# Kernel optimization log

Hardware: AMD Instinct MI355X
Metric: run time of the kernel (lower is better)

The kernel has to match this reference:

```python
import jax, jax.numpy as jnp
import numpy as np

EMB = 1024
HEADS = 16
HEAD_SZ = 64
INNER = 4 * EMB
EPS = 1e-5


def layer_norm(x, g, b):
    mu = jnp.mean(x, axis=-1, keepdims=True)
    var = jnp.mean(jnp.square(x - mu), axis=-1, keepdims=True)
    return (x - mu) * jax.lax.rsqrt(var + EPS) * g + b


def setup_inputs() -> dict:
    key = jax.random.key(0)
    ks = jax.random.split(key, 12)
    s = 1.0 / np.sqrt(EMB)
    si = 1.0 / np.sqrt(INNER)
    return {
        "x": jax.random.normal(ks[0], (4, 2048, EMB), dtype=jnp.float32),
        "Wq": jax.random.uniform(ks[1], (EMB, HEADS * HEAD_SZ), jnp.float32, -s, s),
        "Wk": jax.random.uniform(ks[2], (EMB, HEADS * HEAD_SZ), jnp.float32, -s, s),
        "Wv": jax.random.uniform(ks[3], (EMB, HEADS * HEAD_SZ), jnp.float32, -s, s),
        "Wo": jax.random.uniform(ks[4], (HEADS * HEAD_SZ, EMB), jnp.float32, -s, s),
        "bo": jax.random.uniform(ks[5], (EMB,), jnp.float32, -s, s),
        "g1": jnp.ones((EMB,), jnp.float32),
        "b1": jnp.zeros((EMB,), jnp.float32),
        "W1": jax.random.uniform(ks[6], (EMB, INNER), jnp.float32, -s, s),
        "bf1": jax.random.uniform(ks[7], (INNER,), jnp.float32, -s, s),
        "W2": jax.random.uniform(ks[8], (INNER, EMB), jnp.float32, -si, si),
        "bf2": jax.random.uniform(ks[9], (EMB,), jnp.float32, -si, si),
        "g2": jnp.ones((EMB,), jnp.float32),
        "b2": jnp.zeros((EMB,), jnp.float32),
    }


def reference(x, Wq, Wk, Wv, Wo, bo, g1, b1, W1, bf1, W2, bf2, g2, b2):
    bs, seq, _ = x.shape
    # QKV projections -> [b, h, s, d]
    def split_heads(t):
        return t.reshape(bs, seq, HEADS, HEAD_SZ).transpose(0, 2, 1, 3)
    q = split_heads(x @ Wq)
    k = split_heads(x @ Wk)
    v = split_heads(x @ Wv)
    # scaled dot-product attention (vanilla, no mask; pdrop=0)
    attn = jnp.einsum("bhqd,bhkd->bhqk", q, k) / np.sqrt(HEAD_SZ)
    attn = jax.nn.softmax(attn, axis=-1)
    out = jnp.einsum("bhqk,bhkd->bhqd", attn, v)
    out = out.transpose(0, 2, 1, 3).reshape(bs, seq, HEADS * HEAD_SZ)
    out = out @ Wo + bo
    # residual + post-LN
    h = layer_norm(x + out, g1, b1)
    # FFN
    ff = jax.nn.relu(h @ W1 + bf1) @ W2 + bf2
    return layer_norm(h + ff, g2, b2)
```

## Files before the change

kernel.cpp:

```cpp
#include <hip/hip_runtime.h>
#include <stdint.h>

#define DEVI __device__ __forceinline__

typedef __attribute__((ext_vector_type(8))) short bf16x8;
typedef __attribute__((ext_vector_type(4))) short bf16x4;
typedef __attribute__((ext_vector_type(4))) float f32x4;
typedef unsigned short u16;
typedef uint32_t u32;

constexpr int EMB = 1024, SEQ = 2048, NTOK = 8192;
constexpr int HEADS = 16, HD = 64, INNER = 4096;

DEVI u16 f2b(float f) {
  u32 u = __float_as_uint(f);
  return (u16)((u + 0x7FFFu + ((u >> 16) & 1u)) >> 16);
}

DEVI u32 pk2(float lo, float hi) {
  u32 r;
  asm("v_cvt_pk_bf16_f32 %0, %1, %2" : "=v"(r) : "v"(lo), "v"(hi));
  return r;
}

DEVI float exp2v(float x) {
  float r;
  asm("v_exp_f32 %0, %1" : "=v"(r) : "v"(x));
  return r;
}

DEVI void gload16(const void* g, void* l) {
  __builtin_amdgcn_global_load_lds(
      (const __attribute__((address_space(1))) void*)g,
      (__attribute__((address_space(3))) void*)l, 16, 0, 0);
}

DEVI int xcd_swz(int bid, int nwg) { return (bid & 7) * (nwg >> 3) + (bid >> 3); }

__global__ __launch_bounds__(256) void k_cvt(const float* __restrict__ src,
                                             u16* __restrict__ dst, int n4) {
  int i = blockIdx.x * 256 + threadIdx.x;
  if (i >= n4) return;
  float4 v = ((const float4*)src)[i];
  ushort4 o = {f2b(v.x), f2b(v.y), f2b(v.z), f2b(v.w)};
  ((ushort4*)dst)[i] = o;
}

__global__ __launch_bounds__(256) void k_cvtT(const float* __restrict__ src,
                                              u16* __restrict__ dst, int K, int N) {
  __shared__ float t[32][33];
  int bk = blockIdx.x % (K >> 5), bn = blockIdx.x / (K >> 5);
  int tx = threadIdx.x & 31, ty = threadIdx.x >> 5;
#pragma unroll
  for (int i = 0; i < 4; i++)
    t[ty + i * 8][tx] = src[(size_t)(bk * 32 + ty + i * 8) * N + bn * 32 + tx];
  __syncthreads();
#pragma unroll
  for (int i = 0; i < 4; i++)
    dst[(size_t)(bn * 32 + ty + i * 8) * K + bk * 32 + tx] = f2b(t[tx][ty + i * 8]);
}

template <int EPI>
__global__ __launch_bounds__(512, 2) void k_gemm3(
    const u16* __restrict__ A, const u16* __restrict__ BT, int M, int N, int K,
    u16* __restrict__ ob0, u16* __restrict__ ob1, u16* __restrict__ ob2,
    float* __restrict__ of0, const float* __restrict__ bias,
    const float* __restrict__ res) {
  __shared__ u16 LDS[3][24576];
  const int tid = threadIdx.x;
  const int lane = tid & 63, w = tid >> 6;
  const int wr = w >> 1, wc = w & 1;
  const int g = lane >> 4, c = lane & 15;
  const int nbx = N >> 7;
  const int bid = xcd_swz(blockIdx.x, gridDim.x);
  const int by = bid / nbx, bx = bid % nbx;
  const int row0 = by << 8, col0 = bx << 7;
  const int NK = K >> 6;

  const f32x4 z4 = {0.f, 0.f, 0.f, 0.f};
  f32x4 acc[4][4];
#pragma unroll
  for (int m = 0; m < 4; m++)
#pragma unroll
    for (int n = 0; n < 4; n++) acc[m][n] = z4;

  auto stage = [&](int t, int buf) {
    const int k0 = t << 6;
    char* base = (char*)&LDS[buf][0];
#pragma unroll
    for (int i = 0; i < 4; i++) {
      int s = tid + (i << 9);
      int r = s >> 3, cb = s & 7;
      gload16(A + (size_t)(row0 + r) * K + (k0 + ((cb ^ (r & 7)) << 3)),
              base + s * 16);
    }
#pragma unroll
    for (int i = 0; i < 2; i++) {
      int s = tid + (i << 9);
      int r = s >> 3, cb = s & 7;
      gload16(BT + (size_t)(col0 + r) * K + (k0 + ((cb ^ (r & 7)) << 3)),
              base + 32768 + s * 16);
    }
  };

  stage(0, 0);
  stage(1, 1);
  for (int t = 0; t < NK; t++) {
    __builtin_amdgcn_sched_barrier(0);
    if (t + 1 < NK)
      asm volatile("s_waitcnt vmcnt(6)" ::: "memory");
    else
      asm volatile("s_waitcnt vmcnt(0)" ::: "memory");
    __builtin_amdgcn_s_barrier();
    __builtin_amdgcn_sched_barrier(0);
    if (t + 2 < NK) stage(t + 2, (t + 2) % 3);
    const char* Ab = (const char*)&LDS[t % 3][0];
    const char* Bb = Ab + 32768;
    __builtin_amdgcn_s_setprio(1);
#pragma unroll
    for (int kk = 0; kk < 2; kk++) {
      bf16x8 af[4], bfr[4];
#pragma unroll
      for (int m = 0; m < 4; m++) {
        int r = wr * 64 + m * 16 + c;
        int off = (r * 128 + kk * 64 + g * 16) ^ ((r & 7) << 4);
        af[m] = *(const bf16x8*)(Ab + off);
      }
#pragma unroll
      for (int n = 0; n < 4; n++) {
        int r = wc * 64 + n * 16 + c;
        int off = (r * 128 + kk * 64 + g * 16) ^ ((r & 7) << 4);
        bfr[n] = *(const bf16x8*)(Bb + off);
      }
#pragma unroll
      for (int m = 0; m < 4; m++)
#pragma unroll
        for (int n = 0; n < 4; n++)
          acc[m][n] =
              __builtin_amdgcn_mfma_f32_16x16x32_bf16(af[m], bfr[n], acc[m][n], 0, 0, 0);
    }
    __builtin_amdgcn_s_setprio(0);
  }

#pragma unroll
  for (int m = 0; m < 4; m++) {
#pragma unroll
    for (int n = 0; n < 4; n++) {
      int ocol = col0 + wc * 64 + n * 16 + c;
      int orow_base = row0 + wr * 64 + m * 16 + 4 * g;
      if constexpr (EPI == 0) {
        int which = ocol >> 10, rem = ocol & 1023;
        int h = rem >> 6, d = rem & 63;
#pragma unroll
        for (int r = 0; r < 4; r++) {
          int orow = orow_base + r;
          int b = orow >> 11, s = orow & 2047;
          int bh = b * HEADS + h;
          float av = acc[m][n][r];
          if (which == 0)
            ob0[((size_t)bh * SEQ + s) * HD + d] = f2b(av * 0.1803368801111244f);
          else if (which == 1)
            ob1[((size_t)bh * SEQ + s) * HD + d] = f2b(av);
          else
            ob2[((size_t)bh * HD + d) * SEQ + s] = f2b(av);
        }
      } else if constexpr (EPI == 1) {
        float bia = bias[ocol];
#pragma unroll
        for (int r = 0; r < 4; r++) {
          int orow = orow_base + r;
          of0[(size_t)orow * N + ocol] =
              acc[m][n][r] + bia + res[(size_t)orow * N + ocol];
        }
      } else if constexpr (EPI == 2) {
        float bia = bias[ocol];
#pragma unroll
        for (int r = 0; r < 4; r++) {
          int orow = orow_base + r;
          float v = acc[m][n][r] + bia;
          ob0[(size_t)orow * N + ocol] = f2b(v > 0.f ? v : 0.f);
        }
      } else {
        float bia = bias[ocol];
#pragma unroll
        for (int r = 0; r < 4; r++) {
          int orow = orow_base + r;
          of0[(size_t)orow * N + ocol] = acc[m][n][r] + bia;
        }
      }
    }
  }
}

__global__ __launch_bounds__(256, 4) void k_attn(const u16* __restrict__ q,
                                                 const u16* __restrict__ kb,
                                                 const u16* __restrict__ vT,
                                                 u16* __restrict__ attn) {
  __shared__ u16 Ks[2][64 * 64];
  __shared__ u16 Vs[2][64 * 64];
  const int tid = threadIdx.x, lane = tid & 63, w = tid >> 6;
  const int g = lane >> 4, c = lane & 15;
  const int blk = xcd_swz(blockIdx.x, gridDim.x);
  const int bh = blk >> 5, qb = blk & 31;
  const int b = bh >> 4, h = bh & 15;
  const u16* qh = q + (size_t)bh * SEQ * HD;
  const u16* kh = kb + (size_t)bh * SEQ * HD;
  const u16* vh = vT + (size_t)bh * HD * SEQ;
  const int qr = qb * 64 + w * 16 + c;
  bf16x8 qf0 = *(const bf16x8*)(qh + (size_t)qr * HD + 8 * g);
  bf16x8 qf1 = *(const bf16x8*)(qh + (size_t)qr * HD + 32 + 8 * g);

  const f32x4 z4 = {0.f, 0.f, 0.f, 0.f};
  f32x4 O[4];
#pragma unroll
  for (int m = 0; m < 4; m++) O[m] = z4;
  float mI = -3.0e38f, lI = 0.f;

  auto stage = [&](int kt, int buf) {
    const int kv0 = kt * 64;
#pragma unroll
    for (int i = 0; i < 2; i++) {
      int s = tid + (i << 8);
      int r = s >> 3, cb = s & 7;
      gload16(kh + (size_t)(kv0 + r) * HD + ((cb ^ (r & 7)) << 3),
              (char*)Ks[buf] + s * 16);
    }
#pragma unroll
    for (int i = 0; i < 2; i++) {
      int s = tid + (i << 8);
      int r = s >> 3, cb = s & 7;
      gload16(vh + (size_t)r * SEQ + kv0 + ((cb ^ (r & 7)) << 3),
              (char*)Vs[buf] + s * 16);
    }
  };

  stage(0, 0);
  __syncthreads();
  int cur = 0;
  constexpr int NT = SEQ / 64;
  for (int kt = 0; kt < NT; kt++) {
    if (kt + 1 < NT) stage(kt + 1, cur ^ 1);

    const char* ksb = (const char*)Ks[cur];
    f32x4 sc[4];
    __builtin_amdgcn_s_setprio(1);
#pragma unroll
    for (int m = 0; m < 4; m++) {
      int r = 16 * m + c;
      int sw = (r & 7) << 4;
      bf16x8 kf0 = *(const bf16x8*)(ksb + ((r * 128 + g * 16) ^ sw));
      bf16x8 kf1 = *(const bf16x8*)(ksb + ((r * 128 + 64 + g * 16) ^ sw));
      f32x4 a = z4;
      a = __builtin_amdgcn_mfma_f32_16x16x32_bf16(kf0, qf0, a, 0, 0, 0);
      a = __builtin_amdgcn_mfma_f32_16x16x32_bf16(kf1, qf1, a, 0, 0, 0);
      sc[m] = a;
    }
    __builtin_amdgcn_s_setprio(0);

    float mx = sc[0][0];
#pragma unroll
    for (int m = 0; m < 4; m++)
#pragma unroll
      for (int r = 0; r < 4; r++) mx = fmaxf(mx, sc[m][r]);
    mx = fmaxf(mx, __shfl_xor(mx, 16));
    mx = fmaxf(mx, __shfl_xor(mx, 32));
    if (!__all(mx - mI <= 8.f)) {
      float mNew = fmaxf(mI, mx);
      float alpha = exp2v(mI - mNew);
      lI *= alpha;
#pragma unroll
      for (int m = 0; m < 4; m++)
#pragma unroll
        for (int r = 0; r < 4; r++) O[m][r] *= alpha;
      mI = mNew;
    }
    float p[4][4];
    float rs = 0.f;
#pragma unroll
    for (int m = 0; m < 4; m++)
#pragma unroll
      for (int r = 0; r < 4; r++) {
        p[m][r] = exp2v(sc[m][r] - mI);
        rs += p[m][r];
      }
    rs += __shfl_xor(rs, 16);
    rs += __shfl_xor(rs, 32);
    lI += rs;

    union V8w { bf16x8 v; u32 w4[4]; };
    V8w pa0, pa1;
    pa0.w4[0] = pk2(p[0][0], p[0][1]); pa0.w4[1] = pk2(p[0][2], p[0][3]);
    pa0.w4[2] = pk2(p[1][0], p[1][1]); pa0.w4[3] = pk2(p[1][2], p[1][3]);
    pa1.w4[0] = pk2(p[2][0], p[2][1]); pa1.w4[1] = pk2(p[2][2], p[2][3]);
    pa1.w4[2] = pk2(p[3][0], p[3][1]); pa1.w4[3] = pk2(p[3][2], p[3][3]);

    const char* vsb = (const char*)Vs[cur];
    union V8h { bf16x8 v; bf16x4 h2[2]; };
    __builtin_amdgcn_s_setprio(1);
#pragma unroll
    for (int m = 0; m < 4; m++) {
      int d = 16 * m + c;
      int s7 = d & 7;
      int rb = d * 128 + 8 * (g & 1);
      int ch = g >> 1;
      V8h v0, v1;
      v0.h2[0] = *(const bf16x4*)(vsb + rb + (((ch    ) ^ s7) << 4));
      v0.h2[1] = *(const bf16x4*)(vsb + rb + (((ch + 2) ^ s7) << 4));
      v1.h2[0] = *(const bf16x4*)(vsb + rb + (((ch + 4) ^ s7) << 4));
      v1.h2[1] = *(const bf16x4*)(vsb + rb + (((ch + 6) ^ s7) << 4));
      O[m] = __builtin_amdgcn_mfma_f32_16x16x32_bf16(v0.v, pa0.v, O[m], 0, 0, 0);
      O[m] = __builtin_amdgcn_mfma_f32_16x16x32_bf16(v1.v, pa1.v, O[m], 0, 0, 0);
    }
    __builtin_amdgcn_s_setprio(0);

    __syncthreads();
    cur ^= 1;
  }

  float inv = 1.f / lI;
#pragma unroll
  for (int m = 0; m < 4; m++) {
    ushort4 ov = {f2b(O[m][0] * inv), f2b(O[m][1] * inv),
                  f2b(O[m][2] * inv), f2b(O[m][3] * inv)};
    int col = h * 64 + 16 * m + 4 * g;
    *(ushort4*)(attn + ((size_t)(b * SEQ + qr)) * EMB + col) = ov;
  }
}

__global__ __launch_bounds__(256) void k_ln1(const float* __restrict__ y,
                                             const float* __restrict__ gw,
                                             const float* __restrict__ bw,
                                             float* __restrict__ hf,
                                             u16* __restrict__ hb) {
  const int row = blockIdx.x, tid = threadIdx.x, lane = tid & 63, w = tid >> 6;
  const float4 v = ((const float4*)(y + (size_t)row * EMB))[tid];
  float s = v.x + v.y + v.z + v.w;
  float s2 = v.x * v.x + v.y * v.y + v.z * v.z + v.w * v.w;
#pragma unroll
  for (int m = 1; m < 64; m <<= 1) {
    s += __shfl_xor(s, m);
    s2 += __shfl_xor(s2, m);
  }
  __shared__ float rs_[4], rq_[4];
  if (lane == 0) { rs_[w] = s; rq_[w] = s2; }
  __syncthreads();
  s = rs_[0] + rs_[1] + rs_[2] + rs_[3];
  s2 = rq_[0] + rq_[1] + rq_[2] + rq_[3];
  const float mu = s * (1.f / EMB);
  const float var = s2 * (1.f / EMB) - mu * mu;
  const float rstd = rsqrtf(var + 1e-5f);
  const float4 gg = ((const float4*)gw)[tid];
  const float4 bb = ((const float4*)bw)[tid];
  float4 o;
  o.x = (v.x - mu) * rstd * gg.x + bb.x;
  o.y = (v.y - mu) * rstd * gg.y + bb.y;
  o.z = (v.z - mu) * rstd * gg.z + bb.z;
  o.w = (v.w - mu) * rstd * gg.w + bb.w;
  ((float4*)(hf + (size_t)row * EMB))[tid] = o;
  ushort4 ob = {f2b(o.x), f2b(o.y), f2b(o.z), f2b(o.w)};
  ((ushort4*)(hb + (size_t)row * EMB))[tid] = ob;
}

__global__ __launch_bounds__(256) void k_ln2(const float* __restrict__ hf,
                                             const float* __restrict__ z,
                                             const float* __restrict__ gw,
                                             const float* __restrict__ bw,
                                             float* __restrict__ outp) {
  const int row = blockIdx.x, tid = threadIdx.x, lane = tid & 63, w = tid >> 6;
  float4 v = ((const float4*)(hf + (size_t)row * EMB))[tid];
  const float4 zz = ((const float4*)(z + (size_t)row * EMB))[tid];
  v.x += zz.x; v.y += zz.y; v.z += zz.z; v.w += zz.w;
  float s = v.x + v.y + v.z + v.w;
  float s2 = v.x * v.x + v.y * v.y + v.z * v.z + v.w * v.w;
#pragma unroll
  for (int m = 1; m < 64; m <<= 1) {
    s += __shfl_xor(s, m);
    s2 += __shfl_xor(s2, m);
  }
  __shared__ float rs_[4], rq_[4];
  if (lane == 0) { rs_[w] = s; rq_[w] = s2; }
  __syncthreads();
  s = rs_[0] + rs_[1] + rs_[2] + rs_[3];
  s2 = rq_[0] + rq_[1] + rq_[2] + rq_[3];
  const float mu = s * (1.f / EMB);
  const float var = s2 * (1.f / EMB) - mu * mu;
  const float rstd = rsqrtf(var + 1e-5f);
  const float4 gg = ((const float4*)gw)[tid];
  const float4 bb = ((const float4*)bw)[tid];
  float4 o;
  o.x = (v.x - mu) * rstd * gg.x + bb.x;
  o.y = (v.y - mu) * rstd * gg.y + bb.y;
  o.z = (v.z - mu) * rstd * gg.z + bb.z;
  o.w = (v.w - mu) * rstd * gg.w + bb.w;
  ((float4*)(outp + (size_t)row * EMB))[tid] = o;
}

extern "C" void kernel_launch(void* const* d_in, const int* in_sizes, int n_in,
                              void* d_out, int out_size, void* d_ws, size_t ws_size,
                              hipStream_t stream) {
  const float* x = (const float*)d_in[0];
  const float* Wq = (const float*)d_in[1];
  const float* Wk = (const float*)d_in[2];
  const float* Wv = (const float*)d_in[3];
  const float* Wo = (const float*)d_in[4];
  const float* bo = (const float*)d_in[5];
  const float* g1 = (const float*)d_in[6];
  const float* b1 = (const float*)d_in[7];
  const float* W1 = (const float*)d_in[8];
  const float* bf1 = (const float*)d_in[9];
  const float* W2 = (const float*)d_in[10];
  const float* bf2 = (const float*)d_in[11];
  const float* g2 = (const float*)d_in[12];
  const float* b2 = (const float*)d_in[13];
  float* out = (float*)d_out;

  char* ws = (char*)d_ws;
  size_t off = 0;
  auto alloc = [&](size_t bytes) {
    char* p = ws + off;
    off += (bytes + 255) & ~(size_t)255;
    return p;
  };
  u16* xb = (u16*)alloc((size_t)NTOK * EMB * 2);
  u16* wqkvT = (u16*)alloc((size_t)3072 * 1024 * 2);
  u16* qB = (u16*)alloc((size_t)NTOK * EMB * 2);
  u16* kB = (u16*)alloc((size_t)NTOK * EMB * 2);
  u16* vTB = (u16*)alloc((size_t)NTOK * EMB * 2);
  u16* woT = (u16*)alloc((size_t)1024 * 1024 * 2);
  u16* w1T = (u16*)alloc((size_t)4096 * 1024 * 2);
  u16* w2T = (u16*)alloc((size_t)1024 * 4096 * 2);
  float* y = (float*)alloc((size_t)NTOK * EMB * 4);
  u16* ff1 = (u16*)alloc((size_t)NTOK * INNER * 2);
  u16* attn = xb;
  float* hf = (float*)qB;
  u16* hb = vTB;
  float* z = y;

  k_cvt<<<NTOK * EMB / 4 / 256, 256, 0, stream>>>(x, xb, NTOK * EMB / 4);
  k_cvtT<<<1024, 256, 0, stream>>>(Wq, wqkvT, 1024, 1024);
  k_cvtT<<<1024, 256, 0, stream>>>(Wk, wqkvT + 1048576, 1024, 1024);
  k_cvtT<<<1024, 256, 0, stream>>>(Wv, wqkvT + 2097152, 1024, 1024);
  k_cvtT<<<1024, 256, 0, stream>>>(Wo, woT, 1024, 1024);
  k_cvtT<<<4096, 256, 0, stream>>>(W1, w1T, 1024, 4096);
  k_cvtT<<<4096, 256, 0, stream>>>(W2, w2T, 4096, 1024);
  k_gemm3<0><<<(NTOK / 256) * (3072 / 128), 512, 0, stream>>>(
      xb, wqkvT, NTOK, 3072, 1024, qB, kB, vTB, nullptr, nullptr, nullptr);
  k_attn<<<64 * 32, 256, 0, stream>>>(qB, kB, vTB, attn);
  k_gemm3<1><<<(NTOK / 256) * (1024 / 128), 512, 0, stream>>>(
      attn, woT, NTOK, 1024, 1024, nullptr, nullptr, nullptr, y, bo, x);
  k_ln1<<<NTOK, 256, 0, stream>>>(y, g1, b1, hf, hb);
  k_gemm3<2><<<(NTOK / 256) * (4096 / 128), 512, 0, stream>>>(
      hb, w1T, NTOK, 4096, 1024, ff1, nullptr, nullptr, nullptr, bf1, nullptr);
  k_gemm3<3><<<(NTOK / 256) * (1024 / 128), 512, 0, stream>>>(
      ff1, w2T, NTOK, 1024, 4096, nullptr, nullptr, nullptr, z, bf2, nullptr);
  k_ln2<<<NTOK, 256, 0, stream>>>(hf, z, g2, b2, out);
}
```

Before: 574.1 us.

## Split GEMM k-step into two barrier-phased halves and pre-permute V layout

The GEMM main loop is restructured into two phases per k-tile. Each phase loads half of the B fragments from LDS, issues half of the next tile's global-to-LDS prefetch (A first, then B), and then runs MFMAs between workgroup barriers, in a ping-pong style meant to overlap LDS reads, global loads and matrix math. Separately, the QKV epilogue writes V transposed with a permuted sequence order using 8-byte vector stores, so the attention kernel can read each V operand with a single 16-byte LDS load instead of four 8-byte loads. The added barriers and the extra waitcnt handling increase synchronisation, and the permutation must match exactly what the attention kernel expects.

```diff
diff --git a/kernel.cpp b/kernel.cpp
--- a/kernel.cpp
+++ b/kernel.cpp
@@ -4,7 +4,6 @@
 #define DEVI __device__ __forceinline__
 
 typedef __attribute__((ext_vector_type(8))) short bf16x8;
-typedef __attribute__((ext_vector_type(4))) short bf16x4;
 typedef __attribute__((ext_vector_type(4))) float f32x4;
 typedef unsigned short u16;
 typedef uint32_t u32;
@@ -36,6 +35,11 @@
 }
 
 DEVI int xcd_swz(int bid, int nwg) { return (bid & 7) * (nwg >> 3) + (bid >> 3); }
+
+DEVI int vperm(int k) {
+  int g = (k >> 2) & 3, j = k & 3, s2 = k >> 4;
+  return ((s2 >> 1) << 5) + (g << 3) + ((s2 & 1) << 2) + j;
+}
 
 __global__ __launch_bounds__(256) void k_cvt(const float* __restrict__ src,
                                              u16* __restrict__ dst, int n4) {
@@ -61,7 +65,7 @@
 }
 
 template <int EPI>
-__global__ __launch_bounds__(512, 2) void k_gemm3(
+__global__ __launch_bounds__(512, 2) void k_gemm8(
     const u16* __restrict__ A, const u16* __restrict__ BT, int M, int N, int K,
     u16* __restrict__ ob0, u16* __restrict__ ob1, u16* __restrict__ ob2,
     float* __restrict__ of0, const float* __restrict__ bias,
@@ -84,9 +88,9 @@
 #pragma unroll
     for (int n = 0; n < 4; n++) acc[m][n] = z4;
 
-  auto stage = [&](int t, int buf) {
+  auto stageA = [&](int t) {
     const int k0 = t << 6;
-    char* base = (char*)&LDS[buf][0];
+    char* base = (char*)&LDS[t % 3][0];
 #pragma unroll
     for (int i = 0; i < 4; i++) {
       int s = tid + (i << 9);
@@ -94,52 +98,89 @@
       gload16(A + (size_t)(row0 + r) * K + (k0 + ((cb ^ (r & 7)) << 3)),
               base + s * 16);
     }
+  };
+  auto stageB = [&](int t) {
+    const int k0 = t << 6;
+    char* base = (char*)&LDS[t % 3][0] + 32768;
 #pragma unroll
     for (int i = 0; i < 2; i++) {
       int s = tid + (i << 9);
       int r = s >> 3, cb = s & 7;
       gload16(BT + (size_t)(col0 + r) * K + (k0 + ((cb ^ (r & 7)) << 3)),
-              base + 32768 + s * 16);
+              base + s * 16);
     }
   };
 
-  stage(0, 0);
-  stage(1, 1);
+  stageA(0); stageB(0);
+  stageA(1); stageB(1);
+  asm volatile("s_waitcnt vmcnt(6)" ::: "memory");
+  __builtin_amdgcn_s_barrier();
+
   for (int t = 0; t < NK; t++) {
+    const char* Ab = (const char*)&LDS[t % 3][0];
+    const char* Bb = Ab + 32768;
+
+    bf16x8 af[4][2], bfr[2][2];
+#pragma unroll
+    for (int m = 0; m < 4; m++)
+#pragma unroll
+      for (int kk = 0; kk < 2; kk++) {
+        int r = wr * 64 + m * 16 + c;
+        af[m][kk] = *(const bf16x8*)(Ab + ((r * 128 + kk * 64 + g * 16) ^ ((r & 7) << 4)));
+      }
+#pragma unroll
+    for (int ni = 0; ni < 2; ni++)
+#pragma unroll
+      for (int kk = 0; kk < 2; kk++) {
+        int rb = wc * 64 + ni * 16 + c;
+        bfr[ni][kk] = *(const bf16x8*)(Bb + ((rb * 128 + kk * 64 + g * 16) ^ ((rb & 7) << 4)));
+      }
+    if (t + 2 < NK) stageA(t + 2);
     __builtin_amdgcn_sched_barrier(0);
-    if (t + 1 < NK)
+    __builtin_amdgcn_s_barrier();
+    asm volatile("s_waitcnt lgkmcnt(0)" ::: "memory");
+    __builtin_amdgcn_sched_barrier(0);
+    __builtin_amdgcn_s_setprio(1);
+#pragma unroll
+    for (int m = 0; m < 4; m++)
+#pragma unroll
+      for (int ni = 0; ni < 2; ni++)
+#pragma unroll
+        for (int kk = 0; kk < 2; kk++)
+          acc[m][ni] = __builtin_amdgcn_mfma_f32_16x16x32_bf16(af[m][kk], bfr[ni][kk],
+                                                               acc[m][ni], 0, 0, 0);
+    __builtin_amdgcn_s_setprio(0);
+    __builtin_amdgcn_sched_barrier(0);
+    __builtin_amdgcn_s_barrier();
+
+#pragma unroll
+    for (int ni = 0; ni < 2; ni++)
+#pragma unroll
+      for (int kk = 0; kk < 2; kk++) {
+        int rb = wc * 64 + 32 + ni * 16 + c;
+        bfr[ni][kk] = *(const bf16x8*)(Bb + ((rb * 128 + kk * 64 + g * 16) ^ ((rb & 7) << 4)));
+      }
+    if (t + 2 < NK) stageB(t + 2);
+    __builtin_amdgcn_sched_barrier(0);
+    __builtin_amdgcn_s_barrier();
+    asm volatile("s_waitcnt lgkmcnt(0)" ::: "memory");
+    __builtin_amdgcn_sched_barrier(0);
+    __builtin_amdgcn_s_setprio(1);
+#pragma unroll
+    for (int m = 0; m < 4; m++)
+#pragma unroll
+      for (int ni = 0; ni < 2; ni++)
+#pragma unroll
+        for (int kk = 0; kk < 2; kk++)
+          acc[m][2 + ni] = __builtin_amdgcn_mfma_f32_16x16x32_bf16(af[m][kk], bfr[ni][kk],
+                                                                   acc[m][2 + ni], 0, 0, 0);
+    __builtin_amdgcn_s_setprio(0);
+    __builtin_amdgcn_sched_barrier(0);
+    if (t + 2 < NK)
       asm volatile("s_waitcnt vmcnt(6)" ::: "memory");
-    else
+    else if (t + 1 < NK)
       asm volatile("s_waitcnt vmcnt(0)" ::: "memory");
     __builtin_amdgcn_s_barrier();
-    __builtin_amdgcn_sched_barrier(0);
-    if (t + 2 < NK) stage(t + 2, (t + 2) % 3);
-    const char* Ab = (const char*)&LDS[t % 3][0];
-    const char* Bb = Ab + 32768;
-    __builtin_amdgcn_s_setprio(1);
-#pragma unroll
-    for (int kk = 0; kk < 2; kk++) {
-      bf16x8 af[4], bfr[4];
-#pragma unroll
-      for (int m = 0; m < 4; m++) {
-        int r = wr * 64 + m * 16 + c;
-        int off = (r * 128 + kk * 64 + g * 16) ^ ((r & 7) << 4);
-        af[m] = *(const bf16x8*)(Ab + off);
-      }
-#pragma unroll
-      for (int n = 0; n < 4; n++) {
-        int r = wc * 64 + n * 16 + c;
-        int off = (r * 128 + kk * 64 + g * 16) ^ ((r & 7) << 4);
-        bfr[n] = *(const bf16x8*)(Bb + off);
-      }
-#pragma unroll
-      for (int m = 0; m < 4; m++)
-#pragma unroll
-        for (int n = 0; n < 4; n++)
-          acc[m][n] =
-              __builtin_amdgcn_mfma_f32_16x16x32_bf16(af[m], bfr[n], acc[m][n], 0, 0, 0);
-    }
-    __builtin_amdgcn_s_setprio(0);
   }
 
 #pragma unroll
@@ -151,18 +192,26 @@
       if constexpr (EPI == 0) {
         int which = ocol >> 10, rem = ocol & 1023;
         int h = rem >> 6, d = rem & 63;
-#pragma unroll
-        for (int r = 0; r < 4; r++) {
-          int orow = orow_base + r;
-          int b = orow >> 11, s = orow & 2047;
+        if (which == 2) {
+          int b = orow_base >> 11, sl = orow_base & 2047;
+          int blk = sl & ~63, k4 = sl & 63;
+          int p = vperm(k4);
           int bh = b * HEADS + h;
-          float av = acc[m][n][r];
-          if (which == 0)
-            ob0[((size_t)bh * SEQ + s) * HD + d] = f2b(av * 0.1803368801111244f);
-          else if (which == 1)
-            ob1[((size_t)bh * SEQ + s) * HD + d] = f2b(av);
-          else
-            ob2[((size_t)bh * HD + d) * SEQ + s] = f2b(av);
+          ushort4 vv = {f2b(acc[m][n][0]), f2b(acc[m][n][1]),
+                        f2b(acc[m][n][2]), f2b(acc[m][n][3])};
+          *(ushort4*)(ob2 + ((size_t)bh * HD + d) * SEQ + blk + p) = vv;
+        } else {
+#pragma unroll
+          for (int r = 0; r < 4; r++) {
+            int orow = orow_base + r;
+            int b = orow >> 11, s = orow & 2047;
+            int bh = b * HEADS + h;
+            float av = acc[m][n][r];
+            if (which == 0)
+              ob0[((size_t)bh * SEQ + s) * HD + d] = f2b(av * 0.1803368801111244f);
+            else
+              ob1[((size_t)bh * SEQ + s) * HD + d] = f2b(av);
+          }
         }
       } else if constexpr (EPI == 1) {
         float bia = bias[ocol];
@@ -295,21 +344,15 @@
     pa1.w4[2] = pk2(p[3][0], p[3][1]); pa1.w4[3] = pk2(p[3][2], p[3][3]);
 
     const char* vsb = (const char*)Vs[cur];
-    union V8h { bf16x8 v; bf16x4 h2[2]; };
     __builtin_amdgcn_s_setprio(1);
 #pragma unroll
     for (int m = 0; m < 4; m++) {
       int d = 16 * m + c;
-      int s7 = d & 7;
-      int rb = d * 128 + 8 * (g & 1);
-      int ch = g >> 1;
-      V8h v0, v1;
-      v0.h2[0] = *(const bf16x4*)(vsb + rb + (((ch    ) ^ s7) << 4));
-      v0.h2[1] = *(const bf16x4*)(vsb + rb + (((ch + 2) ^ s7) << 4));
-      v1.h2[0] = *(const bf16x4*)(vsb + rb + (((ch + 4) ^ s7) << 4));
-      v1.h2[1] = *(const bf16x4*)(vsb + rb + (((ch + 6) ^ s7) << 4));
-      O[m] = __builtin_amdgcn_mfma_f32_16x16x32_bf16(v0.v, pa0.v, O[m], 0, 0, 0);
-      O[m] = __builtin_amdgcn_mfma_f32_16x16x32_bf16(v1.v, pa1.v, O[m], 0, 0, 0);
+      int sw = (d & 7) << 4;
+      bf16x8 v0 = *(const bf16x8*)(vsb + ((d * 128 + g * 16) ^ sw));
+      bf16x8 v1 = *(const bf16x8*)(vsb + ((d * 128 + 64 + g * 16) ^ sw));
+      O[m] = __builtin_amdgcn_mfma_f32_16x16x32_bf16(v0, pa0.v, O[m], 0, 0, 0);
+      O[m] = __builtin_amdgcn_mfma_f32_16x16x32_bf16(v1, pa1.v, O[m], 0, 0, 0);
     }
     __builtin_amdgcn_s_setprio(0);
 
@@ -443,15 +486,15 @@
   k_cvtT<<<1024, 256, 0, stream>>>(Wo, woT, 1024, 1024);
   k_cvtT<<<4096, 256, 0, stream>>>(W1, w1T, 1024, 4096);
   k_cvtT<<<4096, 256, 0, stream>>>(W2, w2T, 4096, 1024);
-  k_gemm3<0><<<(NTOK / 256) * (3072 / 128), 512, 0, stream>>>(
+  k_gemm8<0><<<(NTOK / 256) * (3072 / 128), 512, 0, stream>>>(
       xb, wqkvT, NTOK, 3072, 1024, qB, kB, vTB, nullptr, nullptr, nullptr);
   k_attn<<<64 * 32, 256, 0, stream>>>(qB, kB, vTB, attn);
-  k_gemm3<1><<<(NTOK / 256) * (1024 / 128), 512, 0, stream>>>(
+  k_gemm8<1><<<(NTOK / 256) * (1024 / 128), 512, 0, stream>>>(
       attn, woT, NTOK, 1024, 1024, nullptr, nullptr, nullptr, y, bo, x);
   k_ln1<<<NTOK, 256, 0, stream>>>(y, g1, b1, hf, hb);
-  k_gemm3<2><<<(NTOK / 256) * (4096 / 128), 512, 0, stream>>>(
+  k_gemm8<2><<<(NTOK / 256) * (4096 / 128), 512, 0, stream>>>(
       hb, w1T, NTOK, 4096, 1024, ff1, nullptr, nullptr, nullptr, bf1, nullptr);
-  k_gemm3<3><<<(NTOK / 256) * (1024 / 128), 512, 0, stream>>>(
+  k_gemm8<3><<<(NTOK / 256) * (1024 / 128), 512, 0, stream>>>(
       ff1, w2T, NTOK, 1024, 4096, nullptr, nullptr, nullptr, z, bf2, nullptr);
   k_ln2<<<NTOK, 256, 0, stream>>>(hf, z, g2, b2, out);
 }
```

New measurement: 538.6 us. 6.2% less time.
